# Kernel optimization log

Measured on AMD Instinct MI355X. Metric: run time of the kernel, lower is better.

Reference implementation:

```python
import jax, jax.numpy as jnp
import numpy as np

N_NODES = 50000
N_EDGES = 800000
IN_CH = 64
HID = 128
LAST_HID = 256


def setup_inputs() -> dict:
    key = jax.random.key(0)
    ks = jax.random.split(key, 12)
    x = jax.random.normal(ks[0], (N_NODES, IN_CH), dtype=jnp.float32)
    edge_index = jax.random.randint(ks[1], (2, N_EDGES), 0, N_NODES, dtype=jnp.int64)
    s = lambda fan_in: 1.0 / np.sqrt(fan_in)
    return {
        "x": x,
        "edge_index": edge_index,
        # SAGEConv1: lin_l (aggregated neighbors, with bias), lin_r (root, no bias)
        "W1l": jax.random.normal(ks[2], (HID, IN_CH), dtype=jnp.float32) * s(IN_CH),
        "b1l": jnp.zeros((HID,), dtype=jnp.float32),
        "W1r": jax.random.normal(ks[3], (HID, IN_CH), dtype=jnp.float32) * s(IN_CH),
        # SAGEConv2 -> 1 channel
        "W2l": jax.random.normal(ks[4], (1, HID), dtype=jnp.float32) * s(HID),
        "b2l": jnp.zeros((1,), dtype=jnp.float32),
        "W2r": jax.random.normal(ks[5], (1, HID), dtype=jnp.float32) * s(HID),
        # fc1 (LazyLinear bound to N_NODES input features) and fc2
        "fc1_W": jax.random.normal(ks[6], (LAST_HID, N_NODES), dtype=jnp.float32) * s(N_NODES),
        "fc1_b": jnp.zeros((LAST_HID,), dtype=jnp.float32),
        "fc2_W": jax.random.normal(ks[7], (1, LAST_HID), dtype=jnp.float32) * s(LAST_HID),
        "fc2_b": jnp.zeros((1,), dtype=jnp.float32),
    }


def _sage_conv(h, src, dst, Wl, bl, Wr, n_nodes):
    # PyG SAGEConv (mean aggr): out = lin_l(mean_{j in N(i)} x_j) + lin_r(x_i)
    msgs = h[src]  # [E, F] gather of source node features
    summed = jax.ops.segment_sum(msgs, dst, num_segments=n_nodes)  # [N, F]
    deg = jax.ops.segment_sum(jnp.ones((src.shape[0],), h.dtype), dst, num_segments=n_nodes)
    agg = summed / jnp.maximum(deg, 1.0)[:, None]
    return agg @ Wl.T + bl + h @ Wr.T


def reference(x, edge_index, W1l, b1l, W1r, W2l, b2l, W2r, fc1_W, fc1_b, fc2_W, fc2_b):
    n = x.shape[0]
    src, dst = edge_index[0], edge_index[1]
    h = jax.nn.relu(_sage_conv(x, src, dst, W1l, b1l, W1r, n))   # [N, HID]
    h = jax.nn.relu(_sage_conv(h, src, dst, W2l, b2l, W2r, n))   # [N, 1]
    v = h[:, 0]                                                   # [N]
    z = fc1_W @ v + fc1_b                                         # [LAST_HID]
    pred = fc2_W @ z + fc2_b                                      # [1]
    return pred[0]  # scalar (torch.squeeze)
```

## Files before the change

### kernel.cpp

```cpp
#include <hip/hip_runtime.h>

#define N_NODESC 50000
#define N_EDGESC 800000
#define MAXDEG 64

typedef short bf16x8 __attribute__((ext_vector_type(8)));
typedef short short4v __attribute__((ext_vector_type(4)));
typedef float f32x4  __attribute__((ext_vector_type(4)));

__device__ inline unsigned short f2bf(float f) {
    unsigned u = __float_as_uint(f);
    unsigned r = u + 0x7FFFu + ((u >> 16) & 1u);
    return (unsigned short)(r >> 16);
}
__device__ inline float bf2f(unsigned short h) {
    return __uint_as_float(((unsigned)h) << 16);
}

__global__ void kW0_init_pack(const float* __restrict__ W1l, const float* __restrict__ W1r,
                              short* __restrict__ pkhi, short* __restrict__ pklo,
                              int* __restrict__ deg, float* __restrict__ z) {
    int i = blockIdx.x * 256 + threadIdx.x;
    if (i < N_NODESC) deg[i] = 0;
    if (i < 256) z[i] = 0.0f;
    if (blockIdx.x < 4) {
        int ks = blockIdx.x;
        int t  = threadIdx.x;
        int o  = t & 127;
        int h  = t >> 7;
        const float* src = (ks < 2) ? (W1r + o * 64 + ks * 32)
                                    : (W1l + o * 64 + (ks - 2) * 32);
        #pragma unroll
        for (int qi = 0; qi < 2; qi++) {
            int q = 2 * h + qi;
            float4 a = *(const float4*)(src + q * 8);
            float4 b = *(const float4*)(src + q * 8 + 4);
            float v[8] = {a.x, a.y, a.z, a.w, b.x, b.y, b.z, b.w};
            bf16x8 hv, lv;
            #pragma unroll
            for (int j = 0; j < 8; j++) {
                unsigned short hh = f2bf(v[j]);
                hv[j] = (short)hh;
                lv[j] = (short)f2bf(v[j] - bf2f(hh));
            }
            int idx = ((ks * 4 + q) * 128 + o) * 8;
            *(bf16x8*)&pkhi[idx] = hv;
            *(bf16x8*)&pklo[idx] = lv;
        }
    }
}

#define K1_BLOCKS 2048
#define K1_EPB 1563
__global__ void k1_bucket(const int* __restrict__ ei, int* __restrict__ deg,
                          int* __restrict__ bucket) {
    int g   = blockIdx.x & 3;
    int idx = blockIdx.x >> 2;
    int lo = g * (N_NODESC / 4), hi = lo + (N_NODESC / 4);
    int e0 = idx * K1_EPB;
    for (int i = threadIdx.x; i < K1_EPB; i += 256) {
        int e = e0 + i;
        if (e < N_EDGESC) {
            int dst = ei[N_EDGESC + e];
            int src = ei[e];
            if (dst >= lo && dst < hi) {
                int slot = atomicAdd(&deg[dst], 1);
                if (slot < MAXDEG) bucket[dst * MAXDEG + slot] = src;
            }
        }
    }
}

#define K3S 144
#define K3BLK 32

__launch_bounds__(512, 4)
__global__ void k3_fused(const float* __restrict__ x,
                         const int* __restrict__ deg, const int* __restrict__ bucket,
                         const short* __restrict__ pkhi, const short* __restrict__ pklo,
                         const float* __restrict__ b1l,
                         const float* __restrict__ W2l, const float* __restrict__ W2r,
                         float* __restrict__ s_out, float* __restrict__ t_out) {
    __shared__ __align__(16) short sAhi[K3BLK * K3S];
    __shared__ __align__(16) short sAlo[K3BLK * K3S];
    __shared__ float sSp[8][K3BLK], sTp[8][K3BLK];

    int tid = threadIdx.x;
    int lane = tid & 63;
    int wave = tid >> 6;
    int col = lane & 15;
    int quad = lane >> 4;
    int node0 = blockIdx.x * K3BLK;

    float4 sv;
    {
        int n = tid >> 4, kc = tid & 15;
        int node = node0 + n;
        if (node < N_NODESC) {
            sv = *(const float4*)(x + node * 64 + kc * 4);
        } else {
            sv = make_float4(0.f, 0.f, 0.f, 0.f);
        }
    }
    {
        int n = tid >> 4, kc = tid & 15;
        float v[4] = {sv.x, sv.y, sv.z, sv.w};
        short4v hv, lv;
        #pragma unroll
        for (int j = 0; j < 4; j++) {
            unsigned short h = f2bf(v[j]);
            hv[j] = (short)h;
            lv[j] = (short)f2bf(v[j] - bf2f(h));
        }
        *(short4v*)&sAhi[n * K3S + kc * 4] = hv;
        *(short4v*)&sAlo[n * K3S + kc * 4] = lv;
    }

    {
        int base = node0 + wave * 4;
        int dA = 0, bA = 0, dB = 0, bB = 0;
        if (base < N_NODESC)     { dA = deg[base];     bA = bucket[base * MAXDEG + lane]; }
        if (base + 1 < N_NODESC) { dB = deg[base + 1]; bB = bucket[(base + 1) * MAXDEG + lane]; }
        for (int np = 0; np < 2; np++) {
            int nN = base + 2 * np + 2;
            int dA2 = 0, bA2 = 0, dB2 = 0, bB2 = 0;
            if (np < 1) {
                if (nN < N_NODESC)     { dA2 = deg[nN];     bA2 = bucket[nN * MAXDEG + lane]; }
                if (nN + 1 < N_NODESC) { dB2 = deg[nN + 1]; bB2 = bucket[(nN + 1) * MAXDEG + lane]; }
            }
            int cA = min(dA, MAXDEG);
            int cB = min(dB, MAXDEG);
            int kmax = max(cA, cB);
            float4 aA = make_float4(0.f, 0.f, 0.f, 0.f);
            float4 aB = make_float4(0.f, 0.f, 0.f, 0.f);
            for (int k = 0; k < kmax; k += 8) {
                int i0 = k + quad, i1 = k + 4 + quad;
                int a0 = __shfl(bA, i0);
                int a1 = __shfl(bA, i1);
                int b0 = __shfl(bB, i0);
                int b1 = __shfl(bB, i1);
                if (i0 < cA) {
                    float4 v = ((const float4*)(x + a0 * 64))[col];
                    aA.x += v.x; aA.y += v.y; aA.z += v.z; aA.w += v.w;
                }
                if (i1 < cA) {
                    float4 v = ((const float4*)(x + a1 * 64))[col];
                    aA.x += v.x; aA.y += v.y; aA.z += v.z; aA.w += v.w;
                }
                if (i0 < cB) {
                    float4 v = ((const float4*)(x + b0 * 64))[col];
                    aB.x += v.x; aB.y += v.y; aB.z += v.z; aB.w += v.w;
                }
                if (i1 < cB) {
                    float4 v = ((const float4*)(x + b1 * 64))[col];
                    aB.x += v.x; aB.y += v.y; aB.z += v.z; aB.w += v.w;
                }
            }
            #pragma unroll
            for (int m = 16; m <= 32; m <<= 1) {
                aA.x += __shfl_xor(aA.x, m);
                aA.y += __shfl_xor(aA.y, m);
                aA.z += __shfl_xor(aA.z, m);
                aA.w += __shfl_xor(aA.w, m);
                aB.x += __shfl_xor(aB.x, m);
                aB.y += __shfl_xor(aB.y, m);
                aB.z += __shfl_xor(aB.z, m);
                aB.w += __shfl_xor(aB.w, m);
            }
            if (quad == 0) {
                int nlocA = wave * 4 + 2 * np;
                float invA = 1.0f / (float)max(dA, 1);
                float invB = 1.0f / (float)max(dB, 1);
                float vA[4] = {aA.x * invA, aA.y * invA, aA.z * invA, aA.w * invA};
                float vB[4] = {aB.x * invB, aB.y * invB, aB.z * invB, aB.w * invB};
                short4v hvA, lvA, hvB, lvB;
                #pragma unroll
                for (int j = 0; j < 4; j++) {
                    unsigned short hA = f2bf(vA[j]);
                    hvA[j] = (short)hA;
                    lvA[j] = (short)f2bf(vA[j] - bf2f(hA));
                    unsigned short hB = f2bf(vB[j]);
                    hvB[j] = (short)hB;
                    lvB[j] = (short)f2bf(vB[j] - bf2f(hB));
                }
                *(short4v*)&sAhi[nlocA * K3S + 64 + col * 4] = hvA;
                *(short4v*)&sAlo[nlocA * K3S + 64 + col * 4] = lvA;
                *(short4v*)&sAhi[(nlocA + 1) * K3S + 64 + col * 4] = hvB;
                *(short4v*)&sAlo[(nlocA + 1) * K3S + 64 + col * 4] = lvB;
            }
            dA = dA2; bA = bA2; dB = dB2; bB = bB2;
        }
    }

    int o = wave * 16 + col;
    bf16x8 bhi[4], blo[4];
    float bias_r = b1l[o], w2l_r = W2l[o], w2r_r = W2r[o];
    #pragma unroll
    for (int ks = 0; ks < 4; ks++) {
        int idx = ((ks * 4 + quad) * 128 + o) * 8;
        bhi[ks] = *(const bf16x8*)&pkhi[idx];
        blo[ks] = *(const bf16x8*)&pklo[idx];
    }
    __syncthreads();

    f32x4 acc[2];
    acc[0] = (f32x4)0.f;
    acc[1] = (f32x4)0.f;

    #pragma unroll
    for (int ks = 0; ks < 4; ks++) {
        #pragma unroll
        for (int nt = 0; nt < 2; nt++) {
            int off = (nt * 16 + col) * K3S + ks * 32 + quad * 8;
            bf16x8 ah = *(const bf16x8*)&sAhi[off];
            bf16x8 al = *(const bf16x8*)&sAlo[off];
            acc[nt] = __builtin_amdgcn_mfma_f32_16x16x32_bf16(ah, bhi[ks], acc[nt], 0, 0, 0);
            acc[nt] = __builtin_amdgcn_mfma_f32_16x16x32_bf16(al, bhi[ks], acc[nt], 0, 0, 0);
            acc[nt] = __builtin_amdgcn_mfma_f32_16x16x32_bf16(ah, blo[ks], acc[nt], 0, 0, 0);
        }
    }

    #pragma unroll
    for (int nt = 0; nt < 2; nt++) {
        float sp[4], tp[4];
        #pragma unroll
        for (int reg = 0; reg < 4; reg++) {
            float h = fmaxf(acc[nt][reg] + bias_r, 0.f);
            sp[reg] = h * w2l_r;
            tp[reg] = h * w2r_r;
        }
        #pragma unroll
        for (int reg = 0; reg < 4; reg++) {
            #pragma unroll
            for (int m = 1; m <= 8; m <<= 1) {
                sp[reg] += __shfl_xor(sp[reg], m);
                tp[reg] += __shfl_xor(tp[reg], m);
            }
        }
        if (col == 0) {
            int nn = nt * 16 + quad * 4;
            #pragma unroll
            for (int reg = 0; reg < 4; reg++) {
                sSp[wave][nn + reg] = sp[reg];
                sTp[wave][nn + reg] = tp[reg];
            }
        }
    }
    __syncthreads();
    if (tid < K3BLK) {
        int node = node0 + tid;
        if (node < N_NODESC) {
            float ssum = 0.f, tsum = 0.f;
            #pragma unroll
            for (int w = 0; w < 8; w++) { ssum += sSp[w][tid]; tsum += sTp[w][tid]; }
            s_out[node] = ssum;
            t_out[node] = tsum;
        }
    }
}

__global__ void k4_layer2(const float* __restrict__ s, const float* __restrict__ t,
                          const int* __restrict__ deg, const int* __restrict__ bucket,
                          const float* __restrict__ b2l, float* __restrict__ v) {
    int tid = threadIdx.x;
    int lane = tid & 15;
    int node = blockIdx.x * 16 + (tid >> 4);
    int d = deg[node];
    int c = min(d, MAXDEG);
    float sum = 0.f;
    for (int k = lane; k < c; k += 16) sum += s[bucket[node * MAXDEG + k]];
    sum += __shfl_xor(sum, 1);
    sum += __shfl_xor(sum, 2);
    sum += __shfl_xor(sum, 4);
    sum += __shfl_xor(sum, 8);
    if (lane == 0) {
        float h = sum / (float)max(d, 1) + b2l[0] + t[node];
        v[node] = fmaxf(h, 0.f);
    }
}

__global__ void k5_fc1(const float* __restrict__ fc1W, const float* __restrict__ v,
                       float* __restrict__ z) {
    int row = blockIdx.x >> 2;
    int part = blockIdx.x & 3;
    const float4* W4 = (const float4*)(fc1W + row * 50000 + part * 12500);
    const float4* v4 = (const float4*)(v + part * 12500);
    float sum = 0.f;
    for (int i = threadIdx.x; i < 3125; i += 256) {
        float4 w = W4[i], a = v4[i];
        sum += w.x * a.x + w.y * a.y + w.z * a.z + w.w * a.w;
    }
    #pragma unroll
    for (int m = 1; m < 64; m <<= 1) sum += __shfl_xor(sum, m);
    __shared__ float red[4];
    if ((threadIdx.x & 63) == 0) red[threadIdx.x >> 6] = sum;
    __syncthreads();
    if (threadIdx.x == 0) atomicAdd(&z[row], red[0] + red[1] + red[2] + red[3]);
}

__global__ void k6_head(const float* __restrict__ z, const float* __restrict__ fc1b,
                        const float* __restrict__ fc2W, const float* __restrict__ fc2b,
                        float* __restrict__ out) {
    int t = threadIdx.x;
    float val = (z[t] + fc1b[t]) * fc2W[t];
    #pragma unroll
    for (int m = 1; m < 64; m <<= 1) val += __shfl_xor(val, m);
    __shared__ float red[4];
    if ((t & 63) == 0) red[t >> 6] = val;
    __syncthreads();
    if (t == 0) out[0] = red[0] + red[1] + red[2] + red[3] + fc2b[0];
}

extern "C" void kernel_launch(void* const* d_in, const int* in_sizes, int n_in,
                              void* d_out, int out_size, void* d_ws, size_t ws_size,
                              hipStream_t stream) {
    const float* x    = (const float*)d_in[0];
    const int*   ei   = (const int*)d_in[1];
    const float* W1l  = (const float*)d_in[2];
    const float* b1l  = (const float*)d_in[3];
    const float* W1r  = (const float*)d_in[4];
    const float* W2l  = (const float*)d_in[5];
    const float* b2l  = (const float*)d_in[6];
    const float* W2r  = (const float*)d_in[7];
    const float* fc1W = (const float*)d_in[8];
    const float* fc1b = (const float*)d_in[9];
    const float* fc2W = (const float*)d_in[10];
    const float* fc2b = (const float*)d_in[11];
    float* out = (float*)d_out;

    char* ws = (char*)d_ws;
    int*   deg    = (int*)  (ws + 0);
    float* z      = (float*)(ws + 200192);
    int*   bucket = (int*)  (ws + 201216);
    float* s      = (float*)(ws + 13001216);
    float* t      = (float*)(ws + 13201216);
    float* v      = (float*)(ws + 13401216);
    short* pkhi   = (short*)(ws + 13601280);
    short* pklo   = (short*)(ws + 13634048);

    kW0_init_pack<<<196,  256, 0, stream>>>(W1l, W1r, pkhi, pklo, deg, z);
    k1_bucket    <<<K1_BLOCKS, 256, 0, stream>>>(ei, deg, bucket);
    k3_fused     <<<1563, 512, 0, stream>>>(x, deg, bucket, pkhi, pklo, b1l, W2l, W2r, s, t);
    k4_layer2    <<<3125, 256, 0, stream>>>(s, t, deg, bucket, b2l, v);
    k5_fc1       <<<1024, 256, 0, stream>>>(fc1W, v, z);
    k6_head      <<<1,    256, 0, stream>>>(z, fc1b, fc2W, fc2b, out);
}
```

Before: 201.9 us.

## Gather neighbor features from bf16 copy of x with 16-bit bucket indices

New measurement: 206.1 us. +2.1%, slower.

```diff
diff --git a/kernel.cpp b/kernel.cpp
--- a/kernel.cpp
+++ b/kernel.cpp
@@ -17,12 +17,33 @@
     return __uint_as_float(((unsigned)h) << 16);
 }
 
-__global__ void kW0_init_pack(const float* __restrict__ W1l, const float* __restrict__ W1r,
+__global__ void kW0_init_pack(const float* __restrict__ x,
+                              const float* __restrict__ W1l, const float* __restrict__ W1r,
                               short* __restrict__ pkhi, short* __restrict__ pklo,
+                              unsigned short* __restrict__ xb,
                               int* __restrict__ deg, float* __restrict__ z) {
     int i = blockIdx.x * 256 + threadIdx.x;
     if (i < N_NODESC) deg[i] = 0;
     if (i < 256) z[i] = 0.0f;
+
+    int base = i * 16;
+    if (base < N_NODESC * 64) {
+        const float* src = x + base;
+        bf16x8 h0, h1;
+        #pragma unroll
+        for (int j = 0; j < 2; j++) {
+            float4 a = *(const float4*)(src + j * 8);
+            float4 b = *(const float4*)(src + j * 8 + 4);
+            bf16x8& hh = j ? h1 : h0;
+            hh[0] = (short)f2bf(a.x); hh[1] = (short)f2bf(a.y);
+            hh[2] = (short)f2bf(a.z); hh[3] = (short)f2bf(a.w);
+            hh[4] = (short)f2bf(b.x); hh[5] = (short)f2bf(b.y);
+            hh[6] = (short)f2bf(b.z); hh[7] = (short)f2bf(b.w);
+        }
+        *(bf16x8*)(xb + base) = h0;
+        *(bf16x8*)(xb + base + 8) = h1;
+    }
+
     if (blockIdx.x < 4) {
         int ks = blockIdx.x;
         int t  = threadIdx.x;
@@ -51,12 +72,12 @@
 }
 
 #define K1_BLOCKS 2048
-#define K1_EPB 1563
+#define K1_EPB 782
 __global__ void k1_bucket(const int* __restrict__ ei, int* __restrict__ deg,
-                          int* __restrict__ bucket) {
-    int g   = blockIdx.x & 3;
-    int idx = blockIdx.x >> 2;
-    int lo = g * (N_NODESC / 4), hi = lo + (N_NODESC / 4);
+                          unsigned short* __restrict__ bucket) {
+    int g   = blockIdx.x & 1;
+    int idx = blockIdx.x >> 1;
+    int lo = g * (N_NODESC / 2), hi = lo + (N_NODESC / 2);
     int e0 = idx * K1_EPB;
     for (int i = threadIdx.x; i < K1_EPB; i += 256) {
         int e = e0 + i;
@@ -65,7 +86,7 @@
             int src = ei[e];
             if (dst >= lo && dst < hi) {
                 int slot = atomicAdd(&deg[dst], 1);
-                if (slot < MAXDEG) bucket[dst * MAXDEG + slot] = src;
+                if (slot < MAXDEG) bucket[dst * MAXDEG + slot] = (unsigned short)src;
             }
         }
     }
@@ -75,8 +96,8 @@
 #define K3BLK 32
 
 __launch_bounds__(512, 4)
-__global__ void k3_fused(const float* __restrict__ x,
-                         const int* __restrict__ deg, const int* __restrict__ bucket,
+__global__ void k3_fused(const float* __restrict__ x, const unsigned short* __restrict__ xb,
+                         const int* __restrict__ deg, const unsigned short* __restrict__ bucket,
                          const short* __restrict__ pkhi, const short* __restrict__ pklo,
                          const float* __restrict__ b1l,
                          const float* __restrict__ W2l, const float* __restrict__ W2r,
@@ -118,77 +139,73 @@
 
     {
         int base = node0 + wave * 4;
-        int dA = 0, bA = 0, dB = 0, bB = 0;
-        if (base < N_NODESC)     { dA = deg[base];     bA = bucket[base * MAXDEG + lane]; }
-        if (base + 1 < N_NODESC) { dB = deg[base + 1]; bB = bucket[(base + 1) * MAXDEG + lane]; }
-        for (int np = 0; np < 2; np++) {
-            int nN = base + 2 * np + 2;
-            int dA2 = 0, bA2 = 0, dB2 = 0, bB2 = 0;
-            if (np < 1) {
-                if (nN < N_NODESC)     { dA2 = deg[nN];     bA2 = bucket[nN * MAXDEG + lane]; }
-                if (nN + 1 < N_NODESC) { dB2 = deg[nN + 1]; bB2 = bucket[(nN + 1) * MAXDEG + lane]; }
-            }
-            int cA = min(dA, MAXDEG);
-            int cB = min(dB, MAXDEG);
-            int kmax = max(cA, cB);
-            float4 aA = make_float4(0.f, 0.f, 0.f, 0.f);
-            float4 aB = make_float4(0.f, 0.f, 0.f, 0.f);
-            for (int k = 0; k < kmax; k += 8) {
-                int i0 = k + quad, i1 = k + 4 + quad;
-                int a0 = __shfl(bA, i0);
-                int a1 = __shfl(bA, i1);
-                int b0 = __shfl(bB, i0);
-                int b1 = __shfl(bB, i1);
-                if (i0 < cA) {
-                    float4 v = ((const float4*)(x + a0 * 64))[col];
-                    aA.x += v.x; aA.y += v.y; aA.z += v.z; aA.w += v.w;
+        int dd[4], cc[4];
+        int bb[4];
+        #pragma unroll
+        for (int c = 0; c < 4; c++) {
+            int nd = base + c;
+            dd[c] = 0; bb[c] = 0;
+            if (nd < N_NODESC) {
+                dd[c] = deg[nd];
+                bb[c] = (int)bucket[nd * MAXDEG + lane];
+            }
+        }
+        int kmax = 0;
+        #pragma unroll
+        for (int c = 0; c < 4; c++) { cc[c] = min(dd[c], MAXDEG); kmax = max(kmax, cc[c]); }
+
+        float4 av[4];
+        #pragma unroll
+        for (int c = 0; c < 4; c++) av[c] = make_float4(0.f, 0.f, 0.f, 0.f);
+
+        for (int k = 0; k < kmax; k += 8) {
+            int i0 = k + quad, i1 = k + 4 + quad;
+            #pragma unroll
+            for (int c = 0; c < 4; c++) {
+                int s0 = __shfl(bb[c], i0);
+                int s1 = __shfl(bb[c], i1);
+                if (i0 < cc[c]) {
+                    short4v hv_ = *(const short4v*)(xb + s0 * 64 + col * 4);
+                    av[c].x += bf2f((unsigned short)hv_[0]);
+                    av[c].y += bf2f((unsigned short)hv_[1]);
+                    av[c].z += bf2f((unsigned short)hv_[2]);
+                    av[c].w += bf2f((unsigned short)hv_[3]);
                 }
-                if (i1 < cA) {
-                    float4 v = ((const float4*)(x + a1 * 64))[col];
-                    aA.x += v.x; aA.y += v.y; aA.z += v.z; aA.w += v.w;
+                if (i1 < cc[c]) {
+                    short4v hv_ = *(const short4v*)(xb + s1 * 64 + col * 4);
+                    av[c].x += bf2f((unsigned short)hv_[0]);
+                    av[c].y += bf2f((unsigned short)hv_[1]);
+                    av[c].z += bf2f((unsigned short)hv_[2]);
+                    av[c].w += bf2f((unsigned short)hv_[3]);
                 }
-                if (i0 < cB) {
-                    float4 v = ((const float4*)(x + b0 * 64))[col];
-                    aB.x += v.x; aB.y += v.y; aB.z += v.z; aB.w += v.w;
-                }
-                if (i1 < cB) {
-                    float4 v = ((const float4*)(x + b1 * 64))[col];
-                    aB.x += v.x; aB.y += v.y; aB.z += v.z; aB.w += v.w;
-                }
-            }
+            }
+        }
+        #pragma unroll
+        for (int c = 0; c < 4; c++) {
             #pragma unroll
             for (int m = 16; m <= 32; m <<= 1) {
-                aA.x += __shfl_xor(aA.x, m);
-                aA.y += __shfl_xor(aA.y, m);
-                aA.z += __shfl_xor(aA.z, m);
-                aA.w += __shfl_xor(aA.w, m);
-                aB.x += __shfl_xor(aB.x, m);
-                aB.y += __shfl_xor(aB.y, m);
-                aB.z += __shfl_xor(aB.z, m);
-                aB.w += __shfl_xor(aB.w, m);
-            }
-            if (quad == 0) {
-                int nlocA = wave * 4 + 2 * np;
-                float invA = 1.0f / (float)max(dA, 1);
-                float invB = 1.0f / (float)max(dB, 1);
-                float vA[4] = {aA.x * invA, aA.y * invA, aA.z * invA, aA.w * invA};
-                float vB[4] = {aB.x * invB, aB.y * invB, aB.z * invB, aB.w * invB};
-                short4v hvA, lvA, hvB, lvB;
+                av[c].x += __shfl_xor(av[c].x, m);
+                av[c].y += __shfl_xor(av[c].y, m);
+                av[c].z += __shfl_xor(av[c].z, m);
+                av[c].w += __shfl_xor(av[c].w, m);
+            }
+        }
+        if (quad == 0) {
+            #pragma unroll
+            for (int c = 0; c < 4; c++) {
+                int nloc = wave * 4 + c;
+                float inv = 1.0f / (float)max(dd[c], 1);
+                float vv[4] = {av[c].x * inv, av[c].y * inv, av[c].z * inv, av[c].w * inv};
+                short4v hv, lv;
                 #pragma unroll
                 for (int j = 0; j < 4; j++) {
-                    unsigned short hA = f2bf(vA[j]);
-                    hvA[j] = (short)hA;
-                    lvA[j] = (short)f2bf(vA[j] - bf2f(hA));
-                    unsigned short hB = f2bf(vB[j]);
-                    hvB[j] = (short)hB;
-                    lvB[j] = (short)f2bf(vB[j] - bf2f(hB));
+                    unsigned short h = f2bf(vv[j]);
+                    hv[j] = (short)h;
+                    lv[j] = (short)f2bf(vv[j] - bf2f(h));
                 }
-                *(short4v*)&sAhi[nlocA * K3S + 64 + col * 4] = hvA;
-                *(short4v*)&sAlo[nlocA * K3S + 64 + col * 4] = lvA;
-                *(short4v*)&sAhi[(nlocA + 1) * K3S + 64 + col * 4] = hvB;
-                *(short4v*)&sAlo[(nlocA + 1) * K3S + 64 + col * 4] = lvB;
-            }
-            dA = dA2; bA = bA2; dB = dB2; bB = bB2;
+                *(short4v*)&sAhi[nloc * K3S + 64 + col * 4] = hv;
+                *(short4v*)&sAlo[nloc * K3S + 64 + col * 4] = lv;
+            }
         }
     }
 
@@ -260,7 +277,7 @@
 }
 
 __global__ void k4_layer2(const float* __restrict__ s, const float* __restrict__ t,
-                          const int* __restrict__ deg, const int* __restrict__ bucket,
+                          const int* __restrict__ deg, const unsigned short* __restrict__ bucket,
                           const float* __restrict__ b2l, float* __restrict__ v) {
     int tid = threadIdx.x;
     int lane = tid & 15;
@@ -329,18 +346,19 @@
     float* out = (float*)d_out;
 
     char* ws = (char*)d_ws;
-    int*   deg    = (int*)  (ws + 0);
-    float* z      = (float*)(ws + 200192);
-    int*   bucket = (int*)  (ws + 201216);
-    float* s      = (float*)(ws + 13001216);
-    float* t      = (float*)(ws + 13201216);
-    float* v      = (float*)(ws + 13401216);
-    short* pkhi   = (short*)(ws + 13601280);
-    short* pklo   = (short*)(ws + 13634048);
-
-    kW0_init_pack<<<196,  256, 0, stream>>>(W1l, W1r, pkhi, pklo, deg, z);
+    int*            deg    = (int*)           (ws + 0);
+    float*          z      = (float*)         (ws + 200192);
+    unsigned short* bucket = (unsigned short*)(ws + 201216);
+    unsigned short* xb     = (unsigned short*)(ws + 6601216);
+    float*          s      = (float*)         (ws + 13001216);
+    float*          t      = (float*)         (ws + 13201216);
+    float*          v      = (float*)         (ws + 13401216);
+    short*          pkhi   = (short*)         (ws + 13601280);
+    short*          pklo   = (short*)         (ws + 13634048);
+
+    kW0_init_pack<<<782,  256, 0, stream>>>(x, W1l, W1r, pkhi, pklo, xb, deg, z);
     k1_bucket    <<<K1_BLOCKS, 256, 0, stream>>>(ei, deg, bucket);
-    k3_fused     <<<1563, 512, 0, stream>>>(x, deg, bucket, pkhi, pklo, b1l, W2l, W2r, s, t);
+    k3_fused     <<<1563, 512, 0, stream>>>(x, xb, deg, bucket, pkhi, pklo, b1l, W2l, W2r, s, t);
     k4_layer2    <<<3125, 256, 0, stream>>>(s, t, deg, bucket, b2l, v);
     k5_fc1       <<<1024, 256, 0, stream>>>(fc1W, v, z);
     k6_head      <<<1,    256, 0, stream>>>(z, fc1b, fc2W, fc2b, out);
```
